# Performance work log

Hardware: AMD Instinct MI355X
Metric: run time of the kernel (lower is better)

The kernel has to match this reference:

```python
import jax, jax.numpy as jnp
import numpy as np

B, LMAX, NCOND, NHID = 256, 512, 300, 600

def setup_inputs() -> dict:
    key = jax.random.key(0)
    ks = jax.random.split(key, 7)
    x = jax.random.normal(ks[0], (B, NCOND), dtype=jnp.float32)
    context = jax.random.normal(ks[1], (B, LMAX, NCOND), dtype=jnp.float32)
    lengths = jax.random.randint(ks[2], (B,), 0, LMAX, dtype=jnp.int32)
    W1 = jax.random.normal(ks[3], (NCOND, NHID), dtype=jnp.float32) * (1.0 / np.sqrt(NCOND))
    b1 = jax.random.normal(ks[4], (NHID,), dtype=jnp.float32) * 0.02
    Wa = jax.random.normal(ks[5], (NHID, NCOND), dtype=jnp.float32) * (1.0 / np.sqrt(NHID))
    ba = jax.random.normal(ks[6], (NCOND,), dtype=jnp.float32) * 0.02
    return {"x": x, "context": context, "lengths": lengths, "W1": W1, "b1": b1, "Wa": Wa, "ba": ba}

def reference(x, context, lengths, W1, b1, Wa, ba):
    # lengths clamped to >=1 (a ragged context is always non-empty)
    lens = jnp.maximum(lengths, 1)
    # valid-position mask over padded context: [B, L, 1]
    valid = (jnp.arange(LMAX)[None, :] < lens[:, None])[..., None].astype(context.dtype)
    # per-token MLP: relu(ctx @ W1 + b1)  -> [B, L, nhid]
    h = jax.nn.relu(jnp.einsum('blc,ch->blh', context, W1) + b1)
    # masked mean over valid tokens (ragged mean-pool) -> [B, nhid]
    pooled = jnp.sum(h * valid, axis=1) / lens[:, None].astype(context.dtype)
    # sigmoid gate -> [B, ncond], applied to x embeddings
    gate = jax.nn.sigmoid(jnp.einsum('bh,hc->bc', pooled, Wa) + ba)
    return gate * x
```

## Files before the change

kernel.cpp:

```cpp
#include <hip/hip_runtime.h>
#include <math.h>

#define BB     256
#define LMAX   512
#define NCOND  300
#define NHID   600
#define NSEG   8
#define LSEG   64
#define KPAD   320
#define KLDS   328
#define NCOLP  640

typedef short s16x8 __attribute__((ext_vector_type(8)));
typedef float f32x4 __attribute__((ext_vector_type(4)));

__device__ inline unsigned short f2bf(float f) {
    unsigned int x = __float_as_uint(f);
    x += 0x7fffu + ((x >> 16) & 1u);
    return (unsigned short)(x >> 16);
}

__global__ __launch_bounds__(256) void k0_w1t(const float* __restrict__ W1,
                                              unsigned short* __restrict__ w1t) {
    const int idx = blockIdx.x * 256 + threadIdx.x;
    if (idx >= NCOLP * KPAD) return;
    const int n = idx / KPAD;
    const int k = idx - n * KPAD;
    unsigned short v = 0;
    if (n < NHID && k < NCOND) v = f2bf(W1[(size_t)k * NHID + n]);
    w1t[idx] = v;
}

__global__ __launch_bounds__(256, 3) void k1_mfma_pool(
    const float* __restrict__ ctx, const int* __restrict__ lengths,
    const unsigned short* __restrict__ w1t, const float* __restrict__ b1,
    float* __restrict__ partial)
{
    const int b    = blockIdx.x;
    const int s    = blockIdx.y;
    const int ch   = blockIdx.z;
    const int tid  = threadIdx.x;
    const int lane = tid & 63;
    const int wv   = tid >> 6;
    const int ln15 = lane & 15;
    const int kg   = lane >> 4;

    int count = lengths[b]; if (count < 1) count = 1;
    const int l0   = s * LSEG;
    const int nrows = min(count - l0, LSEG);

    __shared__ __align__(16) unsigned short atile[LSEG * KLDS];

    const int colbase = ch * 320 + wv * 80;
    float psum[5] = {0.f, 0.f, 0.f, 0.f, 0.f};

    if (nrows > 0) {
        const int nmt = (nrows + 15) >> 4;

        {
            unsigned int* a32 = (unsigned int*)atile;
            for (int i = tid; i < LSEG * 14; i += 256) {
                const int r = i / 14, d = i - r * 14;
                a32[r * (KLDS / 2) + 150 + d] = 0u;
            }
        }
        {
            const int nvec = nrows * 75;
            for (int i = tid; i < nvec; i += 256) {
                const int r = i / 75, c4 = i - r * 75;
                const float4 v = *(const float4*)(ctx + ((size_t)(b * LMAX + l0 + r)) * NCOND + c4 * 4);
                union { unsigned short us[4]; short4 s4; } u;
                u.us[0] = f2bf(v.x); u.us[1] = f2bf(v.y);
                u.us[2] = f2bf(v.z); u.us[3] = f2bf(v.w);
                *(short4*)(atile + r * KLDS + c4 * 4) = u.s4;
            }
        }
        __syncthreads();

        f32x4 acc[5][4];
#pragma unroll
        for (int nt = 0; nt < 5; ++nt)
#pragma unroll
            for (int mt = 0; mt < 4; ++mt) acc[nt][mt] = (f32x4){0.f, 0.f, 0.f, 0.f};

        const unsigned short* arow = atile + ln15 * KLDS + kg * 8;
        const unsigned short* brow = w1t + (size_t)(colbase + ln15) * KPAD + kg * 8;

        for (int kc = 0; kc < 10; ++kc) {
            s16x8 af[4];
#pragma unroll
            for (int mt = 0; mt < 4; ++mt)
                if (mt < nmt)
                    af[mt] = *(const s16x8*)(arow + mt * 16 * KLDS + kc * 32);
#pragma unroll
            for (int nt = 0; nt < 5; ++nt) {
                const s16x8 bf = *(const s16x8*)(brow + nt * 16 * KPAD + kc * 32);
#pragma unroll
                for (int mt = 0; mt < 4; ++mt)
                    if (mt < nmt)
                        acc[nt][mt] = __builtin_amdgcn_mfma_f32_16x16x32_bf16(af[mt], bf, acc[nt][mt], 0, 0, 0);
            }
        }

#pragma unroll
        for (int nt = 0; nt < 5; ++nt) {
            const int colg = colbase + nt * 16 + ln15;
            const float b1c = (colg < NHID) ? b1[colg] : 0.f;
            float ssum = 0.f;
#pragma unroll
            for (int mt = 0; mt < 4; ++mt) {
                if (mt < nmt) {
                    const int rbase = mt * 16 + kg * 4;
#pragma unroll
                    for (int r = 0; r < 4; ++r)
                        if (rbase + r < nrows)
                            ssum += fmaxf(acc[nt][mt][r] + b1c, 0.f);
                }
            }
            ssum += __shfl_xor(ssum, 16, 64);
            ssum += __shfl_xor(ssum, 32, 64);
            psum[nt] = ssum;
        }
    }

    if (kg == 0) {
#pragma unroll
        for (int nt = 0; nt < 5; ++nt) {
            const int colg = colbase + nt * 16 + ln15;
            if (colg < NHID)
                partial[((size_t)s * BB + b) * NHID + colg] = psum[nt];
        }
    }
}

__global__ __launch_bounds__(192) void k2_gate(
    const float* __restrict__ x, const int* __restrict__ lengths,
    const float* __restrict__ partial, const float* __restrict__ Wa,
    const float* __restrict__ ba, float* __restrict__ out)
{
    const int b    = blockIdx.x;
    const int half = blockIdx.y;
    const int tid  = threadIdx.x;

    int count = lengths[b]; if (count < 1) count = 1;
    const float inv = 1.0f / (float)count;

    __shared__ float pooled[NHID];
    for (int h = tid; h < NHID; h += 192) {
        float ssum = 0.f;
#pragma unroll
        for (int sp = 0; sp < NSEG; ++sp)
            ssum += partial[((size_t)sp * BB + b) * NHID + h];
        pooled[h] = ssum * inv;
    }
    __syncthreads();

    if (tid < 150) {
        const int n = half * 150 + tid;
        float a0 = ba[n], a1 = 0.f;
        const float4* p4 = (const float4*)pooled;
        for (int h4 = 0; h4 < NHID / 4; h4 += 2) {
            const float4 pv0 = p4[h4];
            const float4 pv1 = p4[h4 + 1];
            const int hb = h4 * 4;
            a0 = fmaf(pv0.x, Wa[(size_t)(hb + 0) * NCOND + n], a0);
            a0 = fmaf(pv0.y, Wa[(size_t)(hb + 1) * NCOND + n], a0);
            a0 = fmaf(pv0.z, Wa[(size_t)(hb + 2) * NCOND + n], a0);
            a0 = fmaf(pv0.w, Wa[(size_t)(hb + 3) * NCOND + n], a0);
            a1 = fmaf(pv1.x, Wa[(size_t)(hb + 4) * NCOND + n], a1);
            a1 = fmaf(pv1.y, Wa[(size_t)(hb + 5) * NCOND + n], a1);
            a1 = fmaf(pv1.z, Wa[(size_t)(hb + 6) * NCOND + n], a1);
            a1 = fmaf(pv1.w, Wa[(size_t)(hb + 7) * NCOND + n], a1);
        }
        const float acc  = a0 + a1;
        const float gate = 1.0f / (1.0f + expf(-acc));
        out[(size_t)b * NCOND + n] = gate * x[(size_t)b * NCOND + n];
    }
}

extern "C" void kernel_launch(void* const* d_in, const int* in_sizes, int n_in,
                              void* d_out, int out_size, void* d_ws, size_t ws_size,
                              hipStream_t stream)
{
    const float* x       = (const float*)d_in[0];
    const float* ctx     = (const float*)d_in[1];
    const int*   lengths = (const int*)  d_in[2];
    const float* W1      = (const float*)d_in[3];
    const float* b1      = (const float*)d_in[4];
    const float* Wa      = (const float*)d_in[5];
    const float* ba      = (const float*)d_in[6];
    float*       out     = (float*)d_out;

    unsigned short* w1t     = (unsigned short*)d_ws;
    float*          partial = (float*)((char*)d_ws + (size_t)NCOLP * KPAD * sizeof(unsigned short));

    k0_w1t<<<(NCOLP * KPAD + 255) / 256, 256, 0, stream>>>(W1, w1t);
    k1_mfma_pool<<<dim3(BB, NSEG, 2), 256, 0, stream>>>(ctx, lengths, w1t, b1, partial);
    k2_gate<<<dim3(BB, 2), 192, 0, stream>>>(x, lengths, partial, Wa, ba, out);
}
```

Measured before the change: 340.0 us.

## Schedule batches longest-first, loop chunks per block, pre-swizzle W1 for MFMA

Replaces the fixed 8-segment grid (many empty blocks plus a partial-sum buffer) with one block per (batch, column-half) that loops over 64-row chunks. Batches are sorted by length in a prep kernel so the longest run first. W1 is pre-swizzled into the MFMA fragment layout for coalesced loads, and A/B fragments are double-buffered across k-steps. The mean is finalized in k1, which removes the partial reduction in k2. The trade-off is less parallelism per batch, so long sequences are processed serially within a single block, and padded rows in the last chunk still run MFMAs.

```diff
diff --git a/kernel.cpp b/kernel.cpp
--- a/kernel.cpp
+++ b/kernel.cpp
@@ -5,11 +5,12 @@
 #define LMAX   512
 #define NCOND  300
 #define NHID   600
-#define NSEG   8
-#define LSEG   64
 #define KPAD   320
 #define KLDS   328
 #define NCOLP  640
+#define NTILE  40
+#define NKC    10
+#define CHUNK  64
 
 typedef short s16x8 __attribute__((ext_vector_type(8)));
 typedef float f32x4 __attribute__((ext_vector_type(4)));
@@ -20,25 +21,46 @@
     return (unsigned short)(x >> 16);
 }
 
-__global__ __launch_bounds__(256) void k0_w1t(const float* __restrict__ W1,
-                                              unsigned short* __restrict__ w1t) {
-    const int idx = blockIdx.x * 256 + threadIdx.x;
-    if (idx >= NCOLP * KPAD) return;
-    const int n = idx / KPAD;
-    const int k = idx - n * KPAD;
-    unsigned short v = 0;
-    if (n < NHID && k < NCOND) v = f2bf(W1[(size_t)k * NHID + n]);
-    w1t[idx] = v;
-}
-
-__global__ __launch_bounds__(256, 3) void k1_mfma_pool(
+__global__ __launch_bounds__(256) void k0_prep(const float* __restrict__ W1,
+                                               const int* __restrict__ lengths,
+                                               unsigned short* __restrict__ w1t,
+                                               int* __restrict__ sched)
+{
+    if (blockIdx.x < 100) {
+        const int t     = blockIdx.x * 256 + threadIdx.x;
+        const int lane  = t & 63;
+        const int g     = t >> 6;
+        const int ntile = g / NKC;
+        const int kc    = g - ntile * NKC;
+        const int n     = ntile * 16 + (lane & 15);
+        const int kbase = kc * 32 + (lane >> 4) * 8;
+        union { unsigned short us[8]; s16x8 v8; } u;
+#pragma unroll
+        for (int j = 0; j < 8; ++j) {
+            const int k = kbase + j;
+            const float w = (n < NHID && k < NCOND) ? W1[(size_t)k * NHID + n] : 0.f;
+            u.us[j] = f2bf(w);
+        }
+        *(s16x8*)(w1t + (size_t)t * 8) = u.v8;
+    } else {
+        const int i = threadIdx.x;
+        int li = lengths[i]; if (li < 1) li = 1;
+        int rank = 0;
+        for (int j = 0; j < BB; ++j) {
+            int lj = lengths[j]; if (lj < 1) lj = 1;
+            rank += (lj > li) || (lj == li && j < i);
+        }
+        sched[rank] = i;
+    }
+}
+
+__global__ __launch_bounds__(256) void k1_mfma_pool(
     const float* __restrict__ ctx, const int* __restrict__ lengths,
     const unsigned short* __restrict__ w1t, const float* __restrict__ b1,
-    float* __restrict__ partial)
-{
-    const int b    = blockIdx.x;
-    const int s    = blockIdx.y;
-    const int ch   = blockIdx.z;
+    const int* __restrict__ sched, float* __restrict__ pooled)
+{
+    const int b    = sched[blockIdx.x >> 1];
+    const int ch   = blockIdx.x & 1;
     const int tid  = threadIdx.x;
     const int lane = tid & 63;
     const int wv   = tid >> 6;
@@ -46,119 +68,129 @@
     const int kg   = lane >> 4;
 
     int count = lengths[b]; if (count < 1) count = 1;
-    const int l0   = s * LSEG;
-    const int nrows = min(count - l0, LSEG);
-
-    __shared__ __align__(16) unsigned short atile[LSEG * KLDS];
-
-    const int colbase = ch * 320 + wv * 80;
+    const int nchunks = (count + CHUNK - 1) / CHUNK;
+
+    __shared__ __align__(16) unsigned short atile[CHUNK * KLDS];
+
+    const int ntile0 = ch * 20 + wv * 5;
+    const unsigned short* bbase = w1t + ((size_t)ntile0 * NKC * 64 + lane) * 8;
+    const unsigned short* arow  = atile + ln15 * KLDS + kg * 8;
+
+    float b1c[5];
+#pragma unroll
+    for (int nt = 0; nt < 5; ++nt) {
+        const int colg = ch * 320 + wv * 80 + nt * 16 + ln15;
+        b1c[nt] = (colg < NHID) ? b1[colg] : 0.f;
+    }
+
     float psum[5] = {0.f, 0.f, 0.f, 0.f, 0.f};
 
-    if (nrows > 0) {
-        const int nmt = (nrows + 15) >> 4;
-
-        {
-            unsigned int* a32 = (unsigned int*)atile;
-            for (int i = tid; i < LSEG * 14; i += 256) {
-                const int r = i / 14, d = i - r * 14;
-                a32[r * (KLDS / 2) + 150 + d] = 0u;
+    for (int c = 0; c < nchunks; ++c) {
+        const int l0    = c * CHUNK;
+        const int valid = min(count - l0, CHUNK);
+
+#pragma unroll
+        for (int p = 0; p < 10; ++p) {
+            const int i  = p * 256 + tid;
+            const int r  = i / 40;
+            const int c8 = i - r * 40;
+            union { unsigned short us[8]; s16x8 v8; } u;
+            if (r < valid && c8 < 38) {
+                const float* src = ctx + ((size_t)b * LMAX + l0 + r) * NCOND + c8 * 8;
+                const float4 v0 = *(const float4*)src;
+                float4 v1 = make_float4(0.f, 0.f, 0.f, 0.f);
+                if (c8 < 37) v1 = *(const float4*)(src + 4);
+                u.us[0] = f2bf(v0.x); u.us[1] = f2bf(v0.y);
+                u.us[2] = f2bf(v0.z); u.us[3] = f2bf(v0.w);
+                u.us[4] = f2bf(v1.x); u.us[5] = f2bf(v1.y);
+                u.us[6] = f2bf(v1.z); u.us[7] = f2bf(v1.w);
+            } else {
+#pragma unroll
+                for (int j = 0; j < 8; ++j) u.us[j] = 0;
             }
-        }
-        {
-            const int nvec = nrows * 75;
-            for (int i = tid; i < nvec; i += 256) {
-                const int r = i / 75, c4 = i - r * 75;
-                const float4 v = *(const float4*)(ctx + ((size_t)(b * LMAX + l0 + r)) * NCOND + c4 * 4);
-                union { unsigned short us[4]; short4 s4; } u;
-                u.us[0] = f2bf(v.x); u.us[1] = f2bf(v.y);
-                u.us[2] = f2bf(v.z); u.us[3] = f2bf(v.w);
-                *(short4*)(atile + r * KLDS + c4 * 4) = u.s4;
+            *(s16x8*)(atile + r * KLDS + c8 * 8) = u.v8;
+        }
+        __syncthreads();
+
+        f32x4 acc[5][4];
+#pragma unroll
+        for (int nt = 0; nt < 5; ++nt)
+#pragma unroll
+            for (int mt = 0; mt < 4; ++mt) acc[nt][mt] = (f32x4){0.f, 0.f, 0.f, 0.f};
+
+        s16x8 bf[2][5], af[2][4];
+#pragma unroll
+        for (int nt = 0; nt < 5; ++nt) bf[0][nt] = *(const s16x8*)(bbase + nt * 5120);
+#pragma unroll
+        for (int mt = 0; mt < 4; ++mt) af[0][mt] = *(const s16x8*)(arow + mt * 16 * KLDS);
+
+#pragma unroll
+        for (int kc = 0; kc < NKC; ++kc) {
+            const int cur = kc & 1, nxt = cur ^ 1;
+            if (kc < NKC - 1) {
+#pragma unroll
+                for (int nt = 0; nt < 5; ++nt)
+                    bf[nxt][nt] = *(const s16x8*)(bbase + nt * 5120 + (kc + 1) * 512);
+#pragma unroll
+                for (int mt = 0; mt < 4; ++mt)
+                    af[nxt][mt] = *(const s16x8*)(arow + mt * 16 * KLDS + (kc + 1) * 32);
             }
-        }
-        __syncthreads();
-
-        f32x4 acc[5][4];
-#pragma unroll
-        for (int nt = 0; nt < 5; ++nt)
-#pragma unroll
-            for (int mt = 0; mt < 4; ++mt) acc[nt][mt] = (f32x4){0.f, 0.f, 0.f, 0.f};
-
-        const unsigned short* arow = atile + ln15 * KLDS + kg * 8;
-        const unsigned short* brow = w1t + (size_t)(colbase + ln15) * KPAD + kg * 8;
-
-        for (int kc = 0; kc < 10; ++kc) {
-            s16x8 af[4];
-#pragma unroll
-            for (int mt = 0; mt < 4; ++mt)
-                if (mt < nmt)
-                    af[mt] = *(const s16x8*)(arow + mt * 16 * KLDS + kc * 32);
-#pragma unroll
-            for (int nt = 0; nt < 5; ++nt) {
-                const s16x8 bf = *(const s16x8*)(brow + nt * 16 * KPAD + kc * 32);
+#pragma unroll
+            for (int nt = 0; nt < 5; ++nt)
 #pragma unroll
                 for (int mt = 0; mt < 4; ++mt)
-                    if (mt < nmt)
-                        acc[nt][mt] = __builtin_amdgcn_mfma_f32_16x16x32_bf16(af[mt], bf, acc[nt][mt], 0, 0, 0);
-            }
+                    acc[nt][mt] = __builtin_amdgcn_mfma_f32_16x16x32_bf16(
+                        af[cur][mt], bf[cur][nt], acc[nt][mt], 0, 0, 0);
         }
 
 #pragma unroll
         for (int nt = 0; nt < 5; ++nt) {
-            const int colg = colbase + nt * 16 + ln15;
-            const float b1c = (colg < NHID) ? b1[colg] : 0.f;
-            float ssum = 0.f;
+            float s = 0.f;
 #pragma unroll
             for (int mt = 0; mt < 4; ++mt) {
-                if (mt < nmt) {
-                    const int rbase = mt * 16 + kg * 4;
-#pragma unroll
-                    for (int r = 0; r < 4; ++r)
-                        if (rbase + r < nrows)
-                            ssum += fmaxf(acc[nt][mt][r] + b1c, 0.f);
+                const int rbase = mt * 16 + kg * 4;
+#pragma unroll
+                for (int r = 0; r < 4; ++r) {
+                    const float h = fmaxf(acc[nt][mt][r] + b1c[nt], 0.f);
+                    if (rbase + r < valid) s += h;
                 }
             }
-            ssum += __shfl_xor(ssum, 16, 64);
-            ssum += __shfl_xor(ssum, 32, 64);
-            psum[nt] = ssum;
-        }
-    }
-
-    if (kg == 0) {
-#pragma unroll
-        for (int nt = 0; nt < 5; ++nt) {
-            const int colg = colbase + nt * 16 + ln15;
+            psum[nt] += s;
+        }
+        __syncthreads();
+    }
+
+    const float inv = 1.0f / (float)count;
+#pragma unroll
+    for (int nt = 0; nt < 5; ++nt) {
+        float s = psum[nt];
+        s += __shfl_xor(s, 16, 64);
+        s += __shfl_xor(s, 32, 64);
+        if (kg == 0) {
+            const int colg = ch * 320 + wv * 80 + nt * 16 + ln15;
             if (colg < NHID)
-                partial[((size_t)s * BB + b) * NHID + colg] = psum[nt];
-        }
-    }
-}
-
-__global__ __launch_bounds__(192) void k2_gate(
-    const float* __restrict__ x, const int* __restrict__ lengths,
-    const float* __restrict__ partial, const float* __restrict__ Wa,
-    const float* __restrict__ ba, float* __restrict__ out)
-{
-    const int b    = blockIdx.x;
-    const int half = blockIdx.y;
-    const int tid  = threadIdx.x;
-
-    int count = lengths[b]; if (count < 1) count = 1;
-    const float inv = 1.0f / (float)count;
-
-    __shared__ float pooled[NHID];
-    for (int h = tid; h < NHID; h += 192) {
-        float ssum = 0.f;
-#pragma unroll
-        for (int sp = 0; sp < NSEG; ++sp)
-            ssum += partial[((size_t)sp * BB + b) * NHID + h];
-        pooled[h] = ssum * inv;
-    }
+                pooled[(size_t)b * NHID + colg] = s * inv;
+        }
+    }
+}
+
+__global__ __launch_bounds__(320) void k2_gate(
+    const float* __restrict__ x, const float* __restrict__ pooled,
+    const float* __restrict__ Wa, const float* __restrict__ ba,
+    float* __restrict__ out)
+{
+    const int b   = blockIdx.x;
+    const int tid = threadIdx.x;
+
+    __shared__ float pl[NHID];
+    for (int h = tid; h < NHID; h += 320)
+        pl[h] = pooled[(size_t)b * NHID + h];
     __syncthreads();
 
-    if (tid < 150) {
-        const int n = half * 150 + tid;
+    if (tid < NCOND) {
+        const int n = tid;
         float a0 = ba[n], a1 = 0.f;
-        const float4* p4 = (const float4*)pooled;
+        const float4* p4 = (const float4*)pl;
         for (int h4 = 0; h4 < NHID / 4; h4 += 2) {
             const float4 pv0 = p4[h4];
             const float4 pv1 = p4[h4 + 1];
@@ -191,10 +223,11 @@
     const float* ba      = (const float*)d_in[6];
     float*       out     = (float*)d_out;
 
-    unsigned short* w1t     = (unsigned short*)d_ws;
-    float*          partial = (float*)((char*)d_ws + (size_t)NCOLP * KPAD * sizeof(unsigned short));
-
-    k0_w1t<<<(NCOLP * KPAD + 255) / 256, 256, 0, stream>>>(W1, w1t);
-    k1_mfma_pool<<<dim3(BB, NSEG, 2), 256, 0, stream>>>(ctx, lengths, w1t, b1, partial);
-    k2_gate<<<dim3(BB, 2), 192, 0, stream>>>(x, lengths, partial, Wa, ba, out);
-}
+    unsigned short* w1t    = (unsigned short*)d_ws;
+    int*            sched  = (int*)((char*)d_ws + 409600);
+    float*          pooled = (float*)((char*)d_ws + 409600 + 1024);
+
+    k0_prep<<<101, 256, 0, stream>>>(W1, lengths, w1t, sched);
+    k1_mfma_pool<<<512, 256, 0, stream>>>(ctx, lengths, w1t, b1, sched, pooled);
+    k2_gate<<<BB, 320, 0, stream>>>(x, pooled, Wa, ba, out);
+}
```

After: 320.2 us. -5.8%, faster.
